# Kernel tuning notes

Hardware: AMD Instinct MI355X
Metric: run time of the kernel (lower is better)

The kernel has to match this reference:

```python
import jax, jax.numpy as jnp
import numpy as np

B = 64          # batch
N = 256         # input_dim (number of MPS sites / pixels)
BOND = 128      # bond dimension
DF = 2          # feature dimension per pixel
OUT = 10        # output classes
EPS = 1e-12


def _xavier_uniform(key, shape, fan_in, fan_out, gain):
    bound = gain * np.sqrt(6.0 / (fan_in + fan_out))
    return jax.random.uniform(key, shape, jnp.float32, -bound, bound)


def setup_inputs() -> dict:
    key = jax.random.key(0)
    k_x, k_c0, k_cr, k_cl = jax.random.split(key, 4)
    gain = float(np.sqrt(2.0 / (1.0 + 0.01 ** 2)))  # leaky_relu gain
    x = jax.random.uniform(k_x, (B, N), dtype=jnp.float32)  # pixels in [0,1]
    # core 0: (1, DF, BOND); torch fan_in = DF*BOND, fan_out = 1*BOND
    core0 = _xavier_uniform(k_c0, (1, DF, BOND), DF * BOND, BOND, gain)
    # remaining N-1 cores: (BOND, DF, BOND); fan_in = DF*BOND, fan_out = BOND*BOND... torch: fan_in = shape[1]*shape[2] = DF*BOND, fan_out = shape[0]*shape[2] = BOND*BOND? No: fan_out = shape[0]*prod(shape[2:]) = BOND*BOND
    cores = _xavier_uniform(k_cr, (N - 1, BOND, DF, BOND), DF * BOND, BOND * BOND, gain)
    classifier = _xavier_uniform(k_cl, (OUT, BOND), BOND, OUT, gain)
    return {"x": x, "core0": core0, "cores": cores, "classifier": classifier}


def _mps_forward(x, core0, cores, classifier):
    b = x.shape[0]
    H = core0.shape[-1]
    # feature map: pixel v -> (1-v, v)
    feats = jnp.stack([1.0 - x, x], axis=-1)                  # (B, N, DF)
    # contract each core with its pixel feature
    special = jnp.einsum('ldh,bd->blh', core0, feats[:, 0])   # (B, 1, H)
    others = jnp.einsum('nldh,bnd->bnlh', cores, feats[:, 1:])  # (B, N-1, H, H)
    log_norm = jnp.zeros((b,), dtype=x.dtype)

    # log-depth tree contraction; loop bound is static (trace-time)
    while 1 + others.shape[1] > 1:
        # pad the special (1,H) leftmost tensor up to (H,H) with zero rows
        padded = jnp.pad(special, ((0, 0), (0, H - special.shape[1]), (0, 0)))
        full = jnp.concatenate([padded[:, None], others], axis=1)  # (B, K, H, H)
        K = full.shape[1]
        odd = (K % 2 != 0)
        if odd:
            last = full[:, -1]
            full = full[:, :-1]
        s1 = full[:, 0::2]                                    # (B, P, H, H)
        s2 = full[:, 1::2]
        cp = jnp.matmul(s1, s2)                               # (B, P, H, H)
        norms = jnp.maximum(
            jnp.sqrt(jnp.sum(cp * cp, axis=(-2, -1))), EPS)   # (B, P)
        log_norm = log_norm + jnp.sum(jnp.log(norms), axis=1)
        cp = cp / norms[:, :, None, None]
        special = cp[:, 0, 0:1, :]                            # keep only row 0
        others = cp[:, 1:]
        if odd:
            others = jnp.concatenate([others, last[:, None]], axis=1)

    mps_out = special[:, 0, :]                                # (B, H)
    logits = mps_out @ classifier.T + log_norm[:, None]      # (B, OUT)
    return logits


def reference(x, core0, cores, classifier):
    return _mps_forward(x, core0, cores, classifier)
```

## Files before the change

kernel.cpp:

```cpp
#include <hip/hip_runtime.h>
#include <stdint.h>


typedef unsigned short u16;
typedef __attribute__((ext_vector_type(8))) short short8;
typedef __attribute__((ext_vector_type(4))) float f32x4;

#define HP 136

__device__ __forceinline__ u16 f2b(float f) {
  uint32_t u = __builtin_bit_cast(uint32_t, f);
  u += 0x7FFFu + ((u >> 16) & 1u);
  return (u16)(u >> 16);
}
__device__ __forceinline__ float b2f(u16 b) {
  uint32_t u = ((uint32_t)b) << 16;
  return __builtin_bit_cast(float, u);
}

struct AccW { f32x4 t[2][2]; };

__device__ __forceinline__ void mfma_w16(const u16* Alds, const u16* Blds,
                                         AccW& acc) {
  const int tid = threadIdx.x;
  const int wid = tid >> 6, lane = tid & 63;
  const int wm = (wid >> 2) * 32, wn = (wid & 3) * 32;
  const int l16 = lane & 15, quad = lane >> 4;
#pragma unroll
  for (int tm = 0; tm < 2; tm++)
#pragma unroll
    for (int tn = 0; tn < 2; tn++)
      acc.t[tm][tn] = (f32x4){0.f, 0.f, 0.f, 0.f};
#pragma unroll
  for (int kk = 0; kk < 128; kk += 32) {
    short8 af[2], bf[2];
#pragma unroll
    for (int t = 0; t < 2; t++) {
      af[t] = *(const short8*)(Alds + (wm + t * 16 + l16) * HP + kk + quad * 8);
      bf[t] = *(const short8*)(Blds + (wn + t * 16 + l16) * HP + kk + quad * 8);
    }
#pragma unroll
    for (int tm = 0; tm < 2; tm++)
#pragma unroll
      for (int tn = 0; tn < 2; tn++)
        acc.t[tm][tn] = __builtin_amdgcn_mfma_f32_16x16x32_bf16(
            af[tm], bf[tn], acc.t[tm][tn], 0, 0, 0);
  }
}

__device__ __forceinline__ float acc_sumsq(const AccW& acc) {
  float ss = 0.f;
#pragma unroll
  for (int tm = 0; tm < 2; tm++)
#pragma unroll
    for (int tn = 0; tn < 2; tn++)
#pragma unroll
      for (int i = 0; i < 4; i++) {
        float v = acc.t[tm][tn][i];
        ss += v * v;
      }
  return ss;
}

__device__ __forceinline__ void bounce_store(u16* Lb, const AccW& acc, float scale,
                                             bool transposed) {
  const int tid = threadIdx.x;
  const int wid = tid >> 6, lane = tid & 63;
  const int wm = (wid >> 2) * 32, wn = (wid & 3) * 32;
  const int l16 = lane & 15, quad = lane >> 4;
#pragma unroll
  for (int tm = 0; tm < 2; tm++)
#pragma unroll
    for (int tn = 0; tn < 2; tn++)
#pragma unroll
      for (int i = 0; i < 4; i++) {
        int r = wm + tm * 16 + quad * 4 + i;
        int c = wn + tn * 16 + l16;
        int key = transposed ? c : r, sec = transposed ? r : c;
        Lb[key * HP + sec] = f2b(acc.t[tm][tn][i] * scale);
      }
}

__device__ __forceinline__ void copy_out(const u16* Lb, u16* out) {
  const int tid = threadIdx.x;
#pragma unroll
  for (int i = 0; i < 2; i++) {
    int g8 = tid + i * 1024;
    int row = g8 >> 4, c8 = g8 & 15;
    *(uint4*)(out + g8 * 8) = *(const uint4*)(Lb + row * HP + c8 * 8);
  }
}

__device__ __forceinline__ void loadM(u16* Lb, const u16* __restrict__ src) {
  const int tid = threadIdx.x;
#pragma unroll
  for (int i = 0; i < 2; i++) {
    int g8 = tid + i * 1024;
    int r = g8 >> 4, c8 = g8 & 15;
    *(uint4*)(Lb + r * HP + c8 * 8) = *(const uint4*)(src + g8 * 8);
  }
}

__device__ __forceinline__ float block_sum(float v, float* red, int nw) {
#pragma unroll
  for (int off = 32; off > 0; off >>= 1) v += __shfl_down(v, off);
  int wid = threadIdx.x >> 6;
  if ((threadIdx.x & 63) == 0) red[wid] = v;
  __syncthreads();
  if (threadIdx.x == 0) {
    float s = 0.f;
    for (int w = 0; w < nw; w++) s += red[w];
    red[0] = s;
  }
  __syncthreads();
  float s = red[0];
  __syncthreads();
  return s;
}

__device__ __forceinline__ float bsum16(float v, float* red) {
#pragma unroll
  for (int off = 32; off > 0; off >>= 1) v += __shfl_down(v, off);
  if ((threadIdx.x & 63) == 0) red[threadIdx.x >> 6] = v;
  __syncthreads();
  float s = 0.f;
#pragma unroll
  for (int w = 0; w < 16; w++) s += red[w];
  return s;
}

__global__ __launch_bounds__(1024) void k1(const float* __restrict__ cores,
                                           u16* __restrict__ T) {
  __shared__ u16 Ald[128 * HP], B0[128 * HP], B1[128 * HP];
  const int j = blockIdx.x;
  const int p = blockIdx.y;
  const float* c1 = cores + (size_t)(2 * j + 1) * 32768;
  const float* c2 = cores + (size_t)(2 * j + 2) * 32768;
  const int tid = threadIdx.x;
#pragma unroll 4
  for (int i = 0; i < 16; i++) {
    int lh = tid + i * 1024;
    int l = lh >> 7, h = lh & 127;
    float a0 = c1[(l * 2 + 0) * 128 + h];
    float av = p ? (c1[(l * 2 + 1) * 128 + h] - a0) : a0;
    Ald[l * HP + h] = f2b(av);
    float b0 = c2[(l * 2 + 0) * 128 + h];
    float b1 = c2[(l * 2 + 1) * 128 + h];
    B0[h * HP + l] = f2b(b0);
    B1[h * HP + l] = f2b(b1 - b0);
  }
  __syncthreads();
  const bool tr = (j % 2) == 0;
  u16* Tj = T + ((size_t)j * 4 + p * 2) * 16384;
  AccW q0, q1;
  mfma_w16(Ald, B0, q0);
  mfma_w16(Ald, B1, q1);
  __syncthreads();
  bounce_store(Ald, q0, 1.f, tr); __syncthreads();
  copy_out(Ald, Tj + 0 * 16384);  __syncthreads();
  bounce_store(Ald, q1, 1.f, tr); __syncthreads();
  copy_out(Ald, Tj + 1 * 16384);
}

__global__ __launch_bounds__(1024, 8) void k1b(const u16* __restrict__ T,
                                               u16* __restrict__ TT) {
  __shared__ u16 Ald[128 * HP], Bld[128 * HP];
  const int t = blockIdx.x;
  const int j2 = blockIdx.y;
  const int m1 = 2 * j2 + 1, m2 = 2 * j2 + 2;
  const u16* TA = T + ((size_t)m1 * 4 + (t >> 2)) * 16384;
  const u16* TB = T + ((size_t)m2 * 4 + (t & 3)) * 16384;
  loadM(Ald, TA);
  loadM(Bld, TB);
  __syncthreads();
  AccW acc;
  mfma_w16(Ald, Bld, acc);
  __syncthreads();
  bounce_store(Ald, acc, 1.f, (j2 % 2) == 0);
  __syncthreads();
  copy_out(Ald, TT + ((size_t)j2 * 16 + t) * 16384);
}

__global__ __launch_bounds__(256) void k1c(const u16* __restrict__ TT,
                                           float* __restrict__ Gpart) {
  __shared__ float Gp[1024];
  const int j2 = blockIdx.x, kc = blockIdx.y;
  const int tid = threadIdx.x;
  const int w = tid >> 6, lane = tid & 63;
  const int l16 = lane & 15, quad = lane >> 4;
  const u16* V = TT + (size_t)j2 * 16 * 16384 + (size_t)l16 * 16384;
  const int k0 = kc * 4096 + w * 1024;
  f32x4 acc = (f32x4){0.f, 0.f, 0.f, 0.f};
  for (int kk = k0; kk < k0 + 1024; kk += 32) {
    short8 av = *(const short8*)(V + kk + quad * 8);
    acc = __builtin_amdgcn_mfma_f32_16x16x32_bf16(av, av, acc, 0, 0, 0);
  }
#pragma unroll
  for (int i = 0; i < 4; i++)
    Gp[w * 256 + (quad * 4 + i) * 16 + l16] = acc[i];
  __syncthreads();
  Gpart[((size_t)j2 * 4 + kc) * 256 + tid] =
      Gp[tid] + Gp[256 + tid] + Gp[512 + tid] + Gp[768 + tid];
}

__global__ __launch_bounds__(128) void k2ns(const float* __restrict__ x,
                                            const float* __restrict__ Gpart,
                                            const float* __restrict__ core0,
                                            const float* __restrict__ cores,
                                            const u16* __restrict__ T,
                                            float* __restrict__ cbuf,
                                            float* __restrict__ sA,
                                            float* __restrict__ logs) {
  __shared__ float Gs[256];
  __shared__ float svec[128];
  __shared__ float red[8];
  const int bx = blockIdx.x, tid = threadIdx.x;
  if (bx < 63) {
    const int j2 = bx;
#pragma unroll
    for (int i = 0; i < 2; i++) {
      int t2 = tid + i * 128;
      float s = 0.f;
#pragma unroll
      for (int kc = 0; kc < 4; kc++)
        s += Gpart[((size_t)j2 * 4 + kc) * 256 + t2];
      Gs[t2] = s;
    }
    __syncthreads();
    if (tid < 64) {
      const int b = tid;
      const float* xb = x + b * 256;
      const int m1 = 2 * j2 + 1, m2 = 2 * j2 + 2;
      float a1 = xb[2 * m1 + 2], b1 = xb[2 * m1 + 3];
      float a2 = xb[2 * m2 + 2], b2 = xb[2 * m2 + 3];
      float c1[4] = {1.f, b1, a1, a1 * b1};
      float c2[4] = {1.f, b2, a2, a2 * b2};
      float c[16];
#pragma unroll
      for (int p = 0; p < 4; p++)
#pragma unroll
        for (int q = 0; q < 4; q++) c[p * 4 + q] = c1[p] * c2[q];
      float n2 = 0.f;
#pragma unroll
      for (int t = 0; t < 16; t++) {
        float s = 0.f;
#pragma unroll
        for (int u = 0; u < 16; u++) s += Gs[t * 16 + u] * c[u];
        n2 += c[t] * s;
      }
      float n = fmaxf(sqrtf(n2), 1e-12f);
      logs[b * 127 + 1 + j2] = logf(n);
      float inv = 1.f / n;
#pragma unroll
      for (int t = 0; t < 16; t++)
        cbuf[((size_t)j2 * 64 + b) * 16 + t] = c[t] * inv;
    }
  } else {
    const int b = bx - 63;
    const float* xb = x + b * 256;
    float x0 = xb[0], x1 = xb[1];
    svec[tid] = core0[tid] * (1.f - x0) + core0[128 + tid] * x0;
    __syncthreads();
    float acc1 = 0.f;
    for (int k = 0; k < 128; k++) {
      float m0 = cores[(k * 2 + 0) * 128 + tid];
      float m1 = cores[(k * 2 + 1) * 128 + tid];
      acc1 += svec[k] * (m0 + x1 * (m1 - m0));
    }
    float tot = block_sum(acc1 * acc1, red, 2);
    float n1 = fmaxf(sqrtf(tot), 1e-12f);
    float ln = logf(n1);
    svec[tid] = acc1 / n1;
    __syncthreads();
    float a = xb[2], bb = xb[3], ab = a * bb;
    float acc2 = 0.f;
    for (int k8 = 0; k8 < 16; k8++) {
      union { uint4 v; u16 s[8]; } q00, q01, q10, q11;
      q00.v = *(const uint4*)(T + tid * 128 + k8 * 8);
      q01.v = *(const uint4*)(T + 16384 + tid * 128 + k8 * 8);
      q10.v = *(const uint4*)(T + 32768 + tid * 128 + k8 * 8);
      q11.v = *(const uint4*)(T + 49152 + tid * 128 + k8 * 8);
#pragma unroll
      for (int e = 0; e < 8; e++) {
        float pk = b2f(q00.s[e]) + a * b2f(q10.s[e]) + bb * b2f(q01.s[e]) +
                   ab * b2f(q11.s[e]);
        acc2 += svec[k8 * 8 + e] * pk;
      }
    }
    float tot2 = block_sum(acc2 * acc2, red, 2);
    float n2 = fmaxf(sqrtf(tot2), 1e-12f);
    sA[b * 128 + tid] = acc2 / n2;
    if (tid == 0) logs[b * 127 + 0] = ln + logf(n2);
  }
}

__global__ __launch_bounds__(256, 4) void k2c(const u16* __restrict__ TT,
                                              const float* __restrict__ cbuf,
                                              u16* __restrict__ M0) {
  const int slice = blockIdx.x;
  const int j2 = blockIdx.y;
  const int tid = threadIdx.x;
  const int e0 = slice * 512 + tid * 2;
  float v[16][2];
#pragma unroll
  for (int t = 0; t < 16; t++) {
    union { uint32_t u; u16 s[2]; } q;
    q.u = *(const uint32_t*)(TT + ((size_t)j2 * 16 + t) * 16384 + e0);
    v[t][0] = b2f(q.s[0]);
    v[t][1] = b2f(q.s[1]);
  }
  const float4* cb4 = (const float4*)(cbuf + (size_t)j2 * 1024);
  u16* out = M0 + (size_t)j2 * 16384 + e0;
#pragma unroll 4
  for (int b = 0; b < 64; b++) {
    float4 c0 = cb4[b * 4 + 0];
    float4 c1 = cb4[b * 4 + 1];
    float4 c2 = cb4[b * 4 + 2];
    float4 c3 = cb4[b * 4 + 3];
    float cc[16] = {c0.x, c0.y, c0.z, c0.w, c1.x, c1.y, c1.z, c1.w,
                    c2.x, c2.y, c2.z, c2.w, c3.x, c3.y, c3.z, c3.w};
    float o0 = 0.f, o1 = 0.f;
#pragma unroll
    for (int t = 0; t < 16; t++) {
      o0 += cc[t] * v[t][0];
      o1 += cc[t] * v[t][1];
    }
    union { uint32_t u; u16 s[2]; } r;
    r.s[0] = f2b(o0);
    r.s[1] = f2b(o1);
    *(uint32_t*)(out + (size_t)b * 63 * 16384) = r.u;
  }
}

__global__ __launch_bounds__(1024, 4) void round2x(const u16* __restrict__ In,
                                                   u16* __restrict__ Out,
                                                   const float* __restrict__ sIn,
                                                   float* __restrict__ sOut,
                                                   float* __restrict__ logs,
                                                   int count_in, int count_out,
                                                   int slot0, int slot1) {
  __shared__ u16 L0[128 * HP], L1[128 * HP];
  __shared__ float svf[256];
  __shared__ float red[16];
  const int b = blockIdx.y, p = blockIdx.x, tid = threadIdx.x;
  const u16* base = In + (size_t)b * count_in * 16384;
  if (p == 0) {
    if (tid < 128) svf[tid] = sIn[b * 128 + tid];
    loadM(L0, base + 1 * 16384);
    loadM(L1, base + 2 * 16384);
    __syncthreads();
    float acc0 = 0.f;
    if (tid < 128) {
      for (int k8 = 0; k8 < 16; k8++) {
        union { uint4 v; u16 s[8]; } q;
        q.v = *(const uint4*)(base + tid * 128 + k8 * 8);
#pragma unroll
        for (int e = 0; e < 8; e++) acc0 += svf[k8 * 8 + e] * b2f(q.s[e]);
      }
    }
    AccW accq;
    mfma_w16(L0, L1, accq);
    __syncthreads();
    bounce_store(L0, accq, 1.f, true);
    if (tid < 128) svf[128 + tid] = acc0;
    if (tid == 0) {
      logs[b * 127 + slot0] = 0.f;
      logs[b * 127 + slot0 + 1] = 0.f;
    }
    __syncthreads();
    float acc2 = 0.f;
    if (tid < 128) {
      for (int l = 0; l < 128; l++) acc2 += svf[128 + l] * b2f(L0[tid * HP + l]);
    }
    float t2 = bsum16((tid < 128) ? acc2 * acc2 : 0.f, red);
    float n2 = fmaxf(sqrtf(t2), 1e-12f);
    if (tid == 0) logs[b * 127 + slot1] = logf(n2);
    if (tid < 128) sOut[b * 128 + tid] = acc2 / n2;
  } else {
    const int m = p - 1;
    loadM(L0, base + (size_t)(4 * m + 3) * 16384);
    loadM(L1, base + (size_t)(4 * m + 4) * 16384);
    __syncthreads();
    AccW a1;
    mfma_w16(L0, L1, a1);
    __syncthreads();
    loadM(L0, base + (size_t)(4 * m + 5) * 16384);
    loadM(L1, base + (size_t)(4 * m + 6) * 16384);
    __syncthreads();
    AccW a2;
    mfma_w16(L0, L1, a2);
    __syncthreads();
    bounce_store(L0, a1, 1.f, false);
    bounce_store(L1, a2, 1.f, true);
    if (tid == 0) {
      logs[b * 127 + slot0 + 2 + 2 * m] = 0.f;
      logs[b * 127 + slot0 + 3 + 2 * m] = 0.f;
    }
    __syncthreads();
    AccW a3;
    mfma_w16(L0, L1, a3);
    float t3 = bsum16(acc_sumsq(a3), red);
    float n3 = fmaxf(sqrtf(t3), 1e-12f);
    if (tid == 0) logs[b * 127 + slot1 + 1 + m] = logf(n3);
    bounce_store(L0, a3, 1.f / n3, (m % 2) == 0);
    __syncthreads();
    copy_out(L0, Out + ((size_t)b * count_out + m) * 16384);
  }
}

__global__ __launch_bounds__(1024, 8) void r7f(const u16* __restrict__ In,
                                               const float* __restrict__ sIn,
                                               const float* __restrict__ logs,
                                               const float* __restrict__ cls,
                                               float* __restrict__ out) {
  __shared__ u16 Ald[128 * HP], Bld[128 * HP];
  __shared__ float svec[128], ovec[128], red[16];
  const int b = blockIdx.x, tid = threadIdx.x;
  if (tid < 128) svec[tid] = sIn[b * 128 + tid];
  loadM(Ald, In + ((size_t)b * 3 + 1) * 16384);
  loadM(Bld, In + ((size_t)b * 3 + 2) * 16384);
  __syncthreads();
  AccW acc;
  mfma_w16(Ald, Bld, acc);
  const u16* M0p = In + (size_t)b * 3 * 16384;
  float acc0 = 0.f;
  if (tid < 128) {
    for (int k8 = 0; k8 < 16; k8++) {
      union { uint4 v; u16 s[8]; } q;
      q.v = *(const uint4*)(M0p + tid * 128 + k8 * 8);
#pragma unroll
      for (int e = 0; e < 8; e++) acc0 += svec[k8 * 8 + e] * b2f(q.s[e]);
    }
  }
  __syncthreads();
  bounce_store(Ald, acc, 1.f, true);
  if (tid < 128) ovec[tid] = acc0;
  __syncthreads();
  float acc2 = 0.f;
  if (tid < 128) {
    for (int r = 0; r < 128; r++) acc2 += ovec[r] * b2f(Ald[tid * HP + r]);
  }
  float tot = bsum16((tid < 128) ? acc2 * acc2 : 0.f, red);
  float n = fmaxf(sqrtf(tot), 1e-12f);
  float lg = logf(n);
  if (tid < 128) svec[tid] = acc2 / n;
  __syncthreads();
  if (tid < 10) {
    float a = 0.f;
    for (int h = 0; h < 128; h++) a += svec[h] * cls[tid * 128 + h];
    float L = lg;
    for (int i = 0; i < 124; i++) L += logs[b * 127 + i];
    out[b * 10 + tid] = a + L;
  }
}

extern "C" void kernel_launch(void* const* d_in, const int* in_sizes, int n_in,
                              void* d_out, int out_size, void* d_ws, size_t ws_size,
                              hipStream_t stream) {
  (void)in_sizes; (void)n_in; (void)out_size; (void)ws_size;
  const float* x     = (const float*)d_in[0];
  const float* core0 = (const float*)d_in[1];
  const float* cores = (const float*)d_in[2];
  const float* cls   = (const float*)d_in[3];
  float* out = (float*)d_out;
  char* ws = (char*)d_ws;

  constexpr size_t SZ_T  = (size_t)127 * 4 * 16384 * 2;
  constexpr size_t SZ_A  = (size_t)64 * 31 * 16384 * 2;
  constexpr size_t SZ_M0 = (size_t)64 * 63 * 16384 * 2;

  u16*   T    = (u16*)(ws);
  u16*   TT   = (u16*)(ws + SZ_T);
  u16*   M2   = (u16*)(ws);
  u16*   M0   = (u16*)(ws + SZ_A);
  char*  tail0 = ws + SZ_A + SZ_M0;
  float* Gpart = (float*)(tail0);
  float* cbuf = (float*)(tail0 + 262144);
  float* sA   = (float*)(tail0 + 262144 + 262144);
  float* sB   = (float*)(tail0 + 262144 + 262144 + 32768);
  float* logs = (float*)(tail0 + 262144 + 262144 + 65536);

  k1  <<<dim3(127, 2), 1024, 0, stream>>>(cores, T);
  k1b <<<dim3(16, 63), 1024, 0, stream>>>(T, TT);
  k1c <<<dim3(63, 4), 256, 0, stream>>>(TT, Gpart);
  k2ns<<<dim3(127), 128, 0, stream>>>(x, Gpart, core0, cores, T, cbuf, sA, logs);
  k2c <<<dim3(32, 63), 256, 0, stream>>>(TT, cbuf, M0);
  round2x<<<dim3(16, 64), 1024, 0, stream>>>(M0, M2, sA, sB, logs, 63, 15, 64, 96);
  round2x<<<dim3(4, 64), 1024, 0, stream>>>(M2, M0, sB, sA, logs, 15, 3, 112, 120);
  r7f  <<<dim3(64), 1024, 0, stream>>>(M0, sA, logs, cls, out);
}
```

Measured before the change: 242.1 us.

## Fuse two tree-contraction rounds into one kernel with deeper per-block subtrees

```diff
diff --git a/kernel.cpp b/kernel.cpp
--- a/kernel.cpp
+++ b/kernel.cpp
@@ -332,19 +332,82 @@
   }
 }
 
-__global__ __launch_bounds__(1024, 4) void round2x(const u16* __restrict__ In,
-                                                   u16* __restrict__ Out,
-                                                   const float* __restrict__ sIn,
-                                                   float* __restrict__ sOut,
-                                                   float* __restrict__ logs,
-                                                   int count_in, int count_out,
-                                                   int slot0, int slot1) {
-  __shared__ u16 L0[128 * HP], L1[128 * HP];
+__device__ __forceinline__ AccW subtree3n(const u16* __restrict__ base, int midx,
+                                          u16* L0, u16* L1, float* red,
+                                          float* logs, int b, float& nOut) {
+  loadM(L0, base + (size_t)(4 * midx + 3) * 16384);
+  loadM(L1, base + (size_t)(4 * midx + 4) * 16384);
+  __syncthreads();
+  AccW a1;
+  mfma_w16(L0, L1, a1);
+  __syncthreads();
+  loadM(L0, base + (size_t)(4 * midx + 5) * 16384);
+  loadM(L1, base + (size_t)(4 * midx + 6) * 16384);
+  __syncthreads();
+  AccW a2;
+  mfma_w16(L0, L1, a2);
+  __syncthreads();
+  bounce_store(L0, a1, 1.f, false);
+  bounce_store(L1, a2, 1.f, true);
+  if (threadIdx.x == 0) {
+    logs[b * 127 + 66 + 2 * midx] = 0.f;
+    logs[b * 127 + 67 + 2 * midx] = 0.f;
+  }
+  __syncthreads();
+  AccW a3;
+  mfma_w16(L0, L1, a3);
+  float t = bsum16(acc_sumsq(a3), red);
+  float n = fmaxf(sqrtf(t), 1e-12f);
+  if (threadIdx.x == 0) logs[b * 127 + 97 + midx] = logf(n);
+  nOut = n;
+  return a3;
+}
+
+__global__ __launch_bounds__(1024, 4) void tree(const u16* __restrict__ In,
+                                                u16* __restrict__ Out,
+                                                const float* __restrict__ sIn,
+                                                float* __restrict__ sOut,
+                                                float* __restrict__ logs) {
+  __shared__ u16 L0[128 * HP], L1[128 * HP], L2[128 * HP], L3[128 * HP];
   __shared__ float svf[256];
   __shared__ float red[16];
   const int b = blockIdx.y, p = blockIdx.x, tid = threadIdx.x;
-  const u16* base = In + (size_t)b * count_in * 16384;
-  if (p == 0) {
+  const u16* base = In + (size_t)b * 63 * 16384;
+  if (p < 3) {
+    const int m = p;
+    float n1, n2, n3, n4;
+    AccW t1 = subtree3n(base, 4 * m + 3, L0, L1, red, logs, b, n1);
+    bounce_store(L2, t1, 1.f / n1, false);
+    AccW t2 = subtree3n(base, 4 * m + 4, L0, L1, red, logs, b, n2);
+    bounce_store(L3, t2, 1.f / n2, true);
+    __syncthreads();
+    AccW pa;
+    mfma_w16(L2, L3, pa);
+    __syncthreads();
+    bounce_store(L2, pa, 1.f, false);
+    AccW t3 = subtree3n(base, 4 * m + 5, L0, L1, red, logs, b, n3);
+    bounce_store(L3, t3, 1.f / n3, false);
+    AccW t4 = subtree3n(base, 4 * m + 6, L0, L1, red, logs, b, n4);
+    bounce_store(L0, t4, 1.f / n4, true);
+    if (tid == 0) {
+      logs[b * 127 + 114 + 2 * m] = 0.f;
+      logs[b * 127 + 115 + 2 * m] = 0.f;
+    }
+    __syncthreads();
+    AccW pb;
+    mfma_w16(L3, L0, pb);
+    __syncthreads();
+    bounce_store(L1, pb, 1.f, true);
+    __syncthreads();
+    AccW f;
+    mfma_w16(L2, L1, f);
+    float tF = bsum16(acc_sumsq(f), red);
+    float nF = fmaxf(sqrtf(tF), 1e-12f);
+    if (tid == 0) logs[b * 127 + 121 + m] = logf(nF);
+    bounce_store(L3, f, 1.f / nF, (m % 2) == 0);
+    __syncthreads();
+    copy_out(L3, Out + ((size_t)b * 3 + m) * 16384);
+  } else {
     if (tid < 128) svf[tid] = sIn[b * 128 + tid];
     loadM(L0, base + 1 * 16384);
     loadM(L1, base + 2 * 16384);
@@ -358,53 +421,57 @@
         for (int e = 0; e < 8; e++) acc0 += svf[k8 * 8 + e] * b2f(q.s[e]);
       }
     }
-    AccW accq;
-    mfma_w16(L0, L1, accq);
-    __syncthreads();
-    bounce_store(L0, accq, 1.f, true);
+    AccW q1;
+    mfma_w16(L0, L1, q1);
+    __syncthreads();
+    bounce_store(L0, q1, 1.f, true);
     if (tid < 128) svf[128 + tid] = acc0;
     if (tid == 0) {
-      logs[b * 127 + slot0] = 0.f;
-      logs[b * 127 + slot0 + 1] = 0.f;
+      logs[b * 127 + 64] = 0.f;
+      logs[b * 127 + 65] = 0.f;
     }
     __syncthreads();
     float acc2 = 0.f;
     if (tid < 128) {
       for (int l = 0; l < 128; l++) acc2 += svf[128 + l] * b2f(L0[tid * HP + l]);
     }
-    float t2 = bsum16((tid < 128) ? acc2 * acc2 : 0.f, red);
-    float n2 = fmaxf(sqrtf(t2), 1e-12f);
-    if (tid == 0) logs[b * 127 + slot1] = logf(n2);
-    if (tid < 128) sOut[b * 128 + tid] = acc2 / n2;
-  } else {
-    const int m = p - 1;
-    loadM(L0, base + (size_t)(4 * m + 3) * 16384);
-    loadM(L1, base + (size_t)(4 * m + 4) * 16384);
-    __syncthreads();
-    AccW a1;
-    mfma_w16(L0, L1, a1);
-    __syncthreads();
-    loadM(L0, base + (size_t)(4 * m + 5) * 16384);
-    loadM(L1, base + (size_t)(4 * m + 6) * 16384);
-    __syncthreads();
-    AccW a2;
-    mfma_w16(L0, L1, a2);
-    __syncthreads();
-    bounce_store(L0, a1, 1.f, false);
-    bounce_store(L1, a2, 1.f, true);
+    float t2s = bsum16((tid < 128) ? acc2 * acc2 : 0.f, red);
+    float nv2 = fmaxf(sqrtf(t2s), 1e-12f);
+    if (tid == 0) logs[b * 127 + 96] = logf(nv2);
+    if (tid < 128) svf[tid] = acc2 / nv2;
+    __syncthreads();
+    float n0s, n1s, n2s;
+    AccW s0 = subtree3n(base, 0, L0, L1, red, logs, b, n0s);
+    bounce_store(L2, s0, 1.f / n0s, true);
+    __syncthreads();
+    float acc3 = 0.f;
+    if (tid < 128) {
+      for (int l = 0; l < 128; l++) acc3 += svf[l] * b2f(L2[tid * HP + l]);
+    }
+    if (tid < 128) svf[128 + tid] = acc3;
+    __syncthreads();
+    AccW s1 = subtree3n(base, 1, L0, L1, red, logs, b, n1s);
+    bounce_store(L2, s1, 1.f / n1s, false);
+    AccW s2 = subtree3n(base, 2, L0, L1, red, logs, b, n2s);
+    bounce_store(L3, s2, 1.f / n2s, true);
     if (tid == 0) {
-      logs[b * 127 + slot0 + 2 + 2 * m] = 0.f;
-      logs[b * 127 + slot0 + 3 + 2 * m] = 0.f;
-    }
-    __syncthreads();
-    AccW a3;
-    mfma_w16(L0, L1, a3);
-    float t3 = bsum16(acc_sumsq(a3), red);
-    float n3 = fmaxf(sqrtf(t3), 1e-12f);
-    if (tid == 0) logs[b * 127 + slot1 + 1 + m] = logf(n3);
-    bounce_store(L0, a3, 1.f / n3, (m % 2) == 0);
-    __syncthreads();
-    copy_out(L0, Out + ((size_t)b * count_out + m) * 16384);
+      logs[b * 127 + 112] = 0.f;
+      logs[b * 127 + 113] = 0.f;
+    }
+    __syncthreads();
+    AccW q2;
+    mfma_w16(L2, L3, q2);
+    __syncthreads();
+    bounce_store(L2, q2, 1.f, true);
+    __syncthreads();
+    float acc4 = 0.f;
+    if (tid < 128) {
+      for (int l = 0; l < 128; l++) acc4 += svf[128 + l] * b2f(L2[tid * HP + l]);
+    }
+    float t4s = bsum16((tid < 128) ? acc4 * acc4 : 0.f, red);
+    float nv4 = fmaxf(sqrtf(t4s), 1e-12f);
+    if (tid == 0) logs[b * 127 + 120] = logf(nv4);
+    if (tid < 128) sOut[b * 128 + tid] = acc4 / nv4;
   }
 }
 
@@ -471,7 +538,7 @@
 
   u16*   T    = (u16*)(ws);
   u16*   TT   = (u16*)(ws + SZ_T);
-  u16*   M2   = (u16*)(ws);
+  u16*   M4   = (u16*)(ws);
   u16*   M0   = (u16*)(ws + SZ_A);
   char*  tail0 = ws + SZ_A + SZ_M0;
   float* Gpart = (float*)(tail0);
@@ -485,7 +552,6 @@
   k1c <<<dim3(63, 4), 256, 0, stream>>>(TT, Gpart);
   k2ns<<<dim3(127), 128, 0, stream>>>(x, Gpart, core0, cores, T, cbuf, sA, logs);
   k2c <<<dim3(32, 63), 256, 0, stream>>>(TT, cbuf, M0);
-  round2x<<<dim3(16, 64), 1024, 0, stream>>>(M0, M2, sA, sB, logs, 63, 15, 64, 96);
-  round2x<<<dim3(4, 64), 1024, 0, stream>>>(M2, M0, sB, sA, logs, 15, 3, 112, 120);
-  r7f  <<<dim3(64), 1024, 0, stream>>>(M0, sA, logs, cls, out);
-}
+  tree<<<dim3(4, 64), 1024, 0, stream>>>(M0, M4, sA, sB, logs);
+  r7f <<<dim3(64), 1024, 0, stream>>>(M4, sB, logs, cls, out);
+}
```

Measured after the change: 227.6 us. 6.0% less time.
